# Kernel optimization log

Hardware: AMD Instinct MI355X
Metric: run time of the kernel (lower is better)

## Reference

```python
import jax, jax.numpy as jnp
import numpy as np

EPS = 1e-8  # torch F.cosine_similarity default eps


def setup_inputs() -> dict:
    key = jax.random.key(0)
    k1, k2, k3, k4 = jax.random.split(key, 4)
    U, I, L = 8192, 8192, 256
    # xavier_uniform bound for Embedding weight (fan_in=n, fan_out=L)
    bu = float(np.sqrt(6.0 / (U + L)))
    bi = float(np.sqrt(6.0 / (I + L)))
    user_embed_w = jax.random.uniform(k1, (U, L), jnp.float32, -bu, bu)
    item_embed_w = jax.random.uniform(k2, (I, L), jnp.float32, -bi, bi)
    user_idx = jax.random.randint(k3, (1024,), 0, U, dtype=jnp.int64 if jax.config.jax_enable_x64 else jnp.int32)
    item_idx = jax.random.randint(k4, (1024,), 0, I, dtype=jnp.int64 if jax.config.jax_enable_x64 else jnp.int32)
    return {
        "user_embed_w": user_embed_w,
        "item_embed_w": item_embed_w,
        "user_idx": user_idx,
        "item_idx": item_idx,
        "is_test": 1,
    }


def _cosine_full(u, v):
    # Faithful to F.cosine_similarity(u[:,None], v[None,:], dim=-1) but
    # expressed as normalize + GEMM: (u.v) / (max(|u|,eps)*max(|v|,eps)).
    un = u / jnp.maximum(jnp.linalg.norm(u, axis=-1, keepdims=True), EPS)
    vn = v / jnp.maximum(jnp.linalg.norm(v, axis=-1, keepdims=True), EPS)
    return jnp.einsum("ul,il->ui", un, vn)  # [U, I]


def reference(user_embed_w, item_embed_w, user_idx, item_idx, is_test):
    if is_test:
        return _cosine_full(user_embed_w, item_embed_w)
    # training path: per-pair cosine similarity of user embeddings (note:
    # original code looks up BOTH indices in user_embed, faithfully kept)
    a = user_embed_w[user_idx]
    b = user_embed_w[item_idx]
    num = jnp.sum(a * b, axis=-1)
    den = jnp.maximum(jnp.linalg.norm(a, axis=-1), EPS) * jnp.maximum(
        jnp.linalg.norm(b, axis=-1), EPS
    )
    return (num / den).reshape(-1, 1)
```

## Files before the change

### kernel.cpp

```cpp
#include <hip/hip_runtime.h>
#include <hip/hip_bf16.h>
#include <stdint.h>


#define LDIM 256
#define NROWS 8192
#define NDIM 8192
#define BM 128
#define BN 128
#define BK 32

typedef __bf16 bf16x8 __attribute__((ext_vector_type(8)));
typedef float f32x4 __attribute__((ext_vector_type(4)));

__device__ __forceinline__ unsigned short f2bf_rne(float f) {
  union { float f; uint32_t u; } c;
  c.f = f;
  uint32_t u = c.u;
  u += 0x7FFFu + ((u >> 16) & 1u);
  return (unsigned short)(u >> 16);
}

__global__ __launch_bounds__(256) void normalize_both(
    const float* __restrict__ userw, const float* __restrict__ itemw,
    unsigned short* __restrict__ dst) {
  const int wave = threadIdx.x >> 6;
  const int lane = threadIdx.x & 63;
  const int row = blockIdx.x * 4 + wave;
  const float* src = (row < NROWS)
                         ? userw + (size_t)row * LDIM
                         : itemw + (size_t)(row - NROWS) * LDIM;

  const float4 v = reinterpret_cast<const float4*>(src)[lane];
  float ss = v.x * v.x + v.y * v.y + v.z * v.z + v.w * v.w;
#pragma unroll
  for (int off = 32; off; off >>= 1) ss += __shfl_xor(ss, off, 64);
  const float rn = 1.0f / fmaxf(sqrtf(ss), 1e-8f);

  ushort4 o;
  o.x = f2bf_rne(v.x * rn);
  o.y = f2bf_rne(v.y * rn);
  o.z = f2bf_rne(v.z * rn);
  o.w = f2bf_rne(v.w * rn);
  reinterpret_cast<ushort4*>(dst + (size_t)row * LDIM)[lane] = o;
}

__device__ __forceinline__ void gld_lds16(const __bf16* g, __bf16* l) {
  __builtin_amdgcn_global_load_lds(
      (const __attribute__((address_space(1))) uint32_t*)g,
      (__attribute__((address_space(3))) uint32_t*)l, 16, 0, 0);
}

__global__ __launch_bounds__(256) void cos_gemm(
    const __bf16* __restrict__ A, const __bf16* __restrict__ B,
    float* __restrict__ C) {
  __shared__ __bf16 As[BM][BK];
  __shared__ __bf16 Bs[BN][BK];
  __shared__ float ep[32][132];

  const int tid  = threadIdx.x;
  const int wid  = tid >> 6;
  const int lane = tid & 63;
  const int bn = blockIdx.x;
  const int bm = blockIdx.y;
  const int wr = wid >> 1;
  const int wc = wid & 1;

  const int m0 = (wid << 5) + (lane >> 2);
  const int k0 = (lane & 3) << 3;

  const __bf16* gA = A + (size_t)(bm * BM + m0) * LDIM + k0;
  const __bf16* gB = B + (size_t)(bn * BN + m0) * LDIM + k0;
  __bf16* lA = &As[0][0] + (wid << 10);
  __bf16* lB = &Bs[0][0] + (wid << 10);

  const int fr = lane & 15;
  const int q = lane >> 4;
  const int kq = q << 3;

  f32x4 acc[4][4] = {};

  for (int kt = 0; kt < LDIM / BK; ++kt) {
    const int ko = kt * BK;
#pragma unroll
    for (int c = 0; c < 2; ++c) {
      gld_lds16(gA + (size_t)(c * 16) * LDIM + ko, lA + (c << 9));
      gld_lds16(gB + (size_t)(c * 16) * LDIM + ko, lB + (c << 9));
    }
    __syncthreads();

    bf16x8 af[4], bv[4];
#pragma unroll
    for (int m = 0; m < 4; ++m)
      af[m] = *reinterpret_cast<const bf16x8*>(&As[wr * 64 + m * 16 + fr][kq]);
#pragma unroll
    for (int n = 0; n < 4; ++n)
      bv[n] = *reinterpret_cast<const bf16x8*>(&Bs[wc * 64 + n * 16 + fr][kq]);

#pragma unroll
    for (int m = 0; m < 4; ++m)
#pragma unroll
      for (int n = 0; n < 4; ++n)
        acc[m][n] = __builtin_amdgcn_mfma_f32_16x16x32_bf16(bv[n], af[m],
                                                            acc[m][n], 0, 0, 0);
    __syncthreads();
  }

  float* Cbase = C + (size_t)(bm * BM) * NDIM + bn * BN;
#pragma unroll
  for (int p = 0; p < 4; ++p) {
#pragma unroll
    for (int n = 0; n < 4; ++n)
      *reinterpret_cast<f32x4*>(&ep[wr * 16 + fr][wc * 64 + n * 16 + (q << 2)]) =
          acc[p][n];
    __syncthreads();
#pragma unroll
    for (int s = 0; s < 4; ++s) {
      const int r = s * 8 + (tid >> 5);
      const int grow = ((r >> 4) << 6) + (p << 4) + (r & 15);
      const f32x4 v = *reinterpret_cast<const f32x4*>(&ep[r][(tid & 31) << 2]);
      __builtin_nontemporal_store(
          v, reinterpret_cast<f32x4*>(Cbase + (size_t)grow * NDIM +
                                      ((tid & 31) << 2)));
    }
    __syncthreads();
  }
}

extern "C" void kernel_launch(void* const* d_in, const int* in_sizes, int n_in,
                              void* d_out, int out_size, void* d_ws, size_t ws_size,
                              hipStream_t stream) {
  const float* user_w = (const float*)d_in[0];
  const float* item_w = (const float*)d_in[1];
  float* out = (float*)d_out;

  unsigned short* un = (unsigned short*)d_ws;
  unsigned short* vn = un + (size_t)NROWS * LDIM;

  normalize_both<<<(2 * NROWS) / 4, 256, 0, stream>>>(user_w, item_w, un);

  dim3 grid(NDIM / BN, NDIM / BM);
  cos_gemm<<<grid, 256, 0, stream>>>((const __bf16*)un, (const __bf16*)vn, out);
}
```

Baseline: 72.38 us.

## Enlarge GEMM tile to 256x128 with 512-thread blocks and rework epilogue

Doubles the M tile to 256 rows and the block to 8 waves, so each loaded B tile is reused by twice as many output rows and the grid shrinks by half. Staging loads are remapped so each thread issues two A loads and one B load per k-step. The epilogue now writes one 64-row wave-row group at a time through a larger LDS buffer, with fully coalesced row stores. This trades more LDS and register pressure per block, plus a serialized epilogue, for fewer redundant global loads.

```diff
diff --git a/kernel.cpp b/kernel.cpp
--- a/kernel.cpp
+++ b/kernel.cpp
@@ -6,7 +6,7 @@
 #define LDIM 256
 #define NROWS 8192
 #define NDIM 8192
-#define BM 128
+#define BM 256
 #define BN 128
 #define BK 32
 
@@ -51,12 +51,12 @@
       (__attribute__((address_space(3))) uint32_t*)l, 16, 0, 0);
 }
 
-__global__ __launch_bounds__(256) void cos_gemm(
+__global__ __launch_bounds__(512, 4) void cos_gemm(
     const __bf16* __restrict__ A, const __bf16* __restrict__ B,
     float* __restrict__ C) {
-  __shared__ __bf16 As[BM][BK];
-  __shared__ __bf16 Bs[BN][BK];
-  __shared__ float ep[32][132];
+  __shared__ __bf16 As[BM * BK];
+  __shared__ __bf16 Bs[BN * BK];
+  __shared__ float ep[64][132];
 
   const int tid  = threadIdx.x;
   const int wid  = tid >> 6;
@@ -66,13 +66,12 @@
   const int wr = wid >> 1;
   const int wc = wid & 1;
 
-  const int m0 = (wid << 5) + (lane >> 2);
-  const int k0 = (lane & 3) << 3;
-
-  const __bf16* gA = A + (size_t)(bm * BM + m0) * LDIM + k0;
-  const __bf16* gB = B + (size_t)(bn * BN + m0) * LDIM + k0;
-  __bf16* lA = &As[0][0] + (wid << 10);
-  __bf16* lB = &Bs[0][0] + (wid << 10);
+  const int srow = tid >> 2;
+  const int sk = (tid & 3) << 3;
+  const __bf16* gA = A + (size_t)(bm * BM + srow) * LDIM + sk;
+  const __bf16* gB = B + (size_t)(bn * BN + srow) * LDIM + sk;
+  __bf16* lA = As + tid * 8;
+  __bf16* lB = Bs + tid * 8;
 
   const int fr = lane & 15;
   const int q = lane >> 4;
@@ -82,20 +81,20 @@
 
   for (int kt = 0; kt < LDIM / BK; ++kt) {
     const int ko = kt * BK;
-#pragma unroll
-    for (int c = 0; c < 2; ++c) {
-      gld_lds16(gA + (size_t)(c * 16) * LDIM + ko, lA + (c << 9));
-      gld_lds16(gB + (size_t)(c * 16) * LDIM + ko, lB + (c << 9));
-    }
+    gld_lds16(gA + ko, lA);
+    gld_lds16(gA + (size_t)128 * LDIM + ko, lA + 4096);
+    gld_lds16(gB + ko, lB);
     __syncthreads();
 
     bf16x8 af[4], bv[4];
 #pragma unroll
     for (int m = 0; m < 4; ++m)
-      af[m] = *reinterpret_cast<const bf16x8*>(&As[wr * 64 + m * 16 + fr][kq]);
+      af[m] = *reinterpret_cast<const bf16x8*>(
+          &As[(wr * 64 + m * 16 + fr) * BK + kq]);
 #pragma unroll
     for (int n = 0; n < 4; ++n)
-      bv[n] = *reinterpret_cast<const bf16x8*>(&Bs[wc * 64 + n * 16 + fr][kq]);
+      bv[n] = *reinterpret_cast<const bf16x8*>(
+          &Bs[(wc * 64 + n * 16 + fr) * BK + kq]);
 
 #pragma unroll
     for (int m = 0; m < 4; ++m)
@@ -108,20 +107,24 @@
 
   float* Cbase = C + (size_t)(bm * BM) * NDIM + bn * BN;
 #pragma unroll
-  for (int p = 0; p < 4; ++p) {
+  for (int s = 0; s < 4; ++s) {
+    if (wr == s) {
 #pragma unroll
-    for (int n = 0; n < 4; ++n)
-      *reinterpret_cast<f32x4*>(&ep[wr * 16 + fr][wc * 64 + n * 16 + (q << 2)]) =
-          acc[p][n];
+      for (int m = 0; m < 4; ++m)
+#pragma unroll
+        for (int n = 0; n < 4; ++n)
+          *reinterpret_cast<f32x4*>(
+              &ep[m * 16 + fr][wc * 64 + n * 16 + (q << 2)]) = acc[m][n];
+    }
     __syncthreads();
 #pragma unroll
-    for (int s = 0; s < 4; ++s) {
-      const int r = s * 8 + (tid >> 5);
-      const int grow = ((r >> 4) << 6) + (p << 4) + (r & 15);
-      const f32x4 v = *reinterpret_cast<const f32x4*>(&ep[r][(tid & 31) << 2]);
+    for (int s2 = 0; s2 < 4; ++s2) {
+      const int c = tid + 512 * s2;
+      const int r = c >> 5;
+      const int col = (c & 31) << 2;
+      const f32x4 v = *reinterpret_cast<const f32x4*>(&ep[r][col]);
       __builtin_nontemporal_store(
-          v, reinterpret_cast<f32x4*>(Cbase + (size_t)grow * NDIM +
-                                      ((tid & 31) << 2)));
+          v, reinterpret_cast<f32x4*>(Cbase + (size_t)(s * 64 + r) * NDIM + col));
     }
     __syncthreads();
   }
@@ -140,5 +143,5 @@
   normalize_both<<<(2 * NROWS) / 4, 256, 0, stream>>>(user_w, item_w, un);
 
   dim3 grid(NDIM / BN, NDIM / BM);
-  cos_gemm<<<grid, 256, 0, stream>>>((const __bf16*)un, (const __bf16*)vn, out);
+  cos_gemm<<<grid, 512, 0, stream>>>((const __bf16*)un, (const __bf16*)vn, out);
 }
```

After: 76.92 us. +6.3%, slower.
